# Optimization experiments

Hardware: AMD Instinct MI355X
Metric: run time of the kernel (lower is better)

Reference implementation:

```python
import jax, jax.numpy as jnp
import numpy as np

NEG_INF = -1e30


def setup_inputs() -> dict:
    key = jax.random.key(0)
    k1, k2 = jax.random.split(key)
    B, S, H, D = 2, 2048, 16, 64
    qkv = jax.random.normal(k1, (B, S, 3, H, D), dtype=jnp.float32)
    pos_bias = jax.random.normal(k2, (H, S, S), dtype=jnp.float32)
    return {"qkv": qkv, "pos_bias": pos_bias}


def reference(qkv, pos_bias):
    # qkv: (B, S, 3, H, D); fixed-length path of FlashAttention.forward
    # (key_padding_mask=None, cu_seqlens=None) -> standard per-batch attention
    # with additive per-head positional bias and causal masking.
    B, S, _, H, D = qkv.shape
    q = qkv[:, :, 0]  # (B, S, H, D)
    k = qkv[:, :, 1]
    v = qkv[:, :, 2]
    softmax_scale = 1.0 / jnp.sqrt(jnp.asarray(D, dtype=qkv.dtype))
    # scores: (B, H, S, S)
    scores = jnp.einsum('bshd,bthd->bhst', q, k) * softmax_scale
    scores = scores + pos_bias[None]  # broadcast bias over batch
    # causal mask (query s attends to keys t <= s)
    causal = jnp.tril(jnp.ones((S, S), dtype=bool))
    scores = jnp.where(causal[None, None], scores, NEG_INF)
    attn = jax.nn.softmax(scores, axis=-1)
    # output: (B, S, H, D)
    out = jnp.einsum('bhst,bthd->bshd', attn, v)
    return out
```

## Files before the change

kernel.cpp:

```cpp
#include <hip/hip_runtime.h>

typedef float f32x4 __attribute__((ext_vector_type(4)));
typedef __bf16 bf16x8 __attribute__((ext_vector_type(8)));

#define MFMA16(a, b, c) __builtin_amdgcn_mfma_f32_16x16x32_bf16(a, b, c, 0, 0, 0)

constexpr int S = 2048, H = 16, Dh = 64;
constexpr int BR = 64, BC = 64;
#define NEG_INF_F (-1e30f)

__device__ __forceinline__ void gld16(const __bf16* g, __bf16* l) {
    __builtin_amdgcn_global_load_lds(
        (const __attribute__((address_space(1))) void*)(g),
        (__attribute__((address_space(3))) void*)(l), 16, 0, 0);
}

__global__ __launch_bounds__(256) void prep(const float* __restrict__ qkv,
                                            __bf16* __restrict__ khat,
                                            __bf16* __restrict__ vT)
{
    __shared__ __bf16 vtile[64][72];
    const int tid = threadIdx.x;
    const int bid = blockIdx.x;
    const int tt  = bid & 31;
    const int bh  = bid >> 5;
    const int b   = bh >> 4, h = bh & 15;
    const int t0  = tt * 64;
    const int tr  = tid >> 2, c0 = (tid & 3) * 16;

    const float* kp = qkv + (((size_t)(b * S + t0 + tr) * 3 + 1) * H + h) * Dh + c0;
    const float* vp = qkv + (((size_t)(b * S + t0 + tr) * 3 + 2) * H + h) * Dh + c0;
    f32x4 k0 = *(const f32x4*)(kp + 0), k1 = *(const f32x4*)(kp + 4),
          k2 = *(const f32x4*)(kp + 8), k3 = *(const f32x4*)(kp + 12);
    f32x4 v0 = *(const f32x4*)(vp + 0), v1 = *(const f32x4*)(vp + 4),
          v2 = *(const f32x4*)(vp + 8), v3 = *(const f32x4*)(vp + 12);
    bf16x8 ka, kb, va, vb;
#pragma unroll
    for (int j = 0; j < 4; ++j) {
        ka[j] = (__bf16)k0[j]; ka[4 + j] = (__bf16)k1[j];
        kb[j] = (__bf16)k2[j]; kb[4 + j] = (__bf16)k3[j];
        va[j] = (__bf16)v0[j]; va[4 + j] = (__bf16)v1[j];
        vb[j] = (__bf16)v2[j]; vb[4 + j] = (__bf16)v3[j];
    }
    {
        __bf16* kd = khat + ((size_t)bh * S + t0 + tr) * Dh;
        const int g0 = c0 >> 3, sw = tr & 7;
        *(bf16x8*)(kd + ((( g0    ) ^ sw) << 3)) = ka;
        *(bf16x8*)(kd + (((g0 + 1) ^ sw) << 3)) = kb;
    }
    *(bf16x8*)&vtile[tr][c0]     = va;
    *(bf16x8*)&vtile[tr][c0 + 8] = vb;
    __syncthreads();
    const int d = tid >> 2, tc0 = (tid & 3) * 16;
    bf16x8 x, y;
#pragma unroll
    for (int i = 0; i < 8; ++i) {
        x[i] = vtile[tc0 + i][d];
        y[i] = vtile[tc0 + 8 + i][d];
    }
    __bf16* vd = vT + ((size_t)bh * Dh + d) * S + t0;
    const int h0 = tc0 >> 3, sv = d & 7;
    *(bf16x8*)(vd + ((( h0    ) ^ sv) << 3)) = x;
    *(bf16x8*)(vd + (((h0 + 1) ^ sv) << 3)) = y;
}

__global__ __launch_bounds__(256, 4) void fa_fwd(
    const float* __restrict__ qkv, const float* __restrict__ pb,
    const __bf16* __restrict__ khat, const __bf16* __restrict__ vT,
    float* __restrict__ out)
{
    __shared__ __bf16 klds[64 * 64];
    __shared__ __bf16 vlds[64 * 64];
    __shared__ __bf16 plds[4][16][72];

    const int tid  = threadIdx.x;
    const int wave = tid >> 6;
    const int lane = tid & 63;
    const int quad = lane >> 4;
    const int l16  = lane & 15;

    const int g  = blockIdx.x >> 8;
    const int pp = blockIdx.x & 255;
    const int kk = pp >> 5, hb = pp & 31;
    const int b  = hb & 1, h = hb >> 1;
    const int qt = (g == 0) ? 31 - kk : (g == 1) ? 16 + kk : (g == 2) ? 15 - kk : kk;
    const int q0 = qt * BR;
    const int bh = b * H + h;
    const float scale = 0.125f;

    const int qrow = q0 + wave * 16 + l16;
    const float* qp = qkv + (((size_t)(b * S + qrow) * 3 + 0) * H + h) * Dh;
    bf16x8 qfrag[2];
#pragma unroll
    for (int ks = 0; ks < 2; ++ks) {
        f32x4 a = *(const f32x4*)(qp + ks * 32 + quad * 8);
        f32x4 c = *(const f32x4*)(qp + ks * 32 + quad * 8 + 4);
#pragma unroll
        for (int j = 0; j < 4; ++j) qfrag[ks][j] = (__bf16)a[j];
#pragma unroll
        for (int j = 0; j < 4; ++j) qfrag[ks][4 + j] = (__bf16)c[j];
    }

    const int lrow  = wave * 16 + quad * 4;
    const int myrow = q0 + lrow;
    float l_r[4] = {0.f, 0.f, 0.f, 0.f};
    f32x4 oacc[4];
#pragma unroll
    for (int dt = 0; dt < 4; ++dt) oacc[dt] = (f32x4){0.f, 0.f, 0.f, 0.f};

    const int seg = wave * 2;
    const int lt  = lane >> 3, le = (lane & 7) * 8;
    const __bf16* kg = khat + ((size_t)bh * S + (seg * 8 + lt)) * 64 + le;
    const __bf16* vg = vT   + ((size_t)bh * Dh + seg * 8 + lt) * S + le;
    __bf16* kl = klds + seg * 512;
    __bf16* vl = vlds + seg * 512;

    const float* bb = pb + (size_t)h * S * S + (size_t)myrow * S + l16;
    const int swz = l16 & 7;

    for (int it = 0; it <= qt; ++it) {
        __syncthreads();
        gld16(kg,         kl);
        gld16(kg + 512,   kl + 512);
        gld16(vg,         vl);
        gld16(vg + 8 * S, vl + 512);
        kg += BC * 64; vg += BC;

        float breg[16];
#pragma unroll
        for (int ct = 0; ct < 4; ++ct)
#pragma unroll
            for (int r = 0; r < 4; ++r) breg[ct * 4 + r] = bb[(size_t)r * S + ct * 16];
        bb += BC;
        __syncthreads();

        f32x4 sacc[4];
#pragma unroll
        for (int ct = 0; ct < 4; ++ct) sacc[ct] = (f32x4){0.f, 0.f, 0.f, 0.f};
#pragma unroll
        for (int ct = 0; ct < 4; ++ct) {
#pragma unroll
            for (int ks = 0; ks < 2; ++ks) {
                bf16x8 kf = *(const bf16x8*)&klds[(ct * 16 + l16) * 64 + (((ks * 4 + quad) ^ swz) << 3)];
                sacc[ct] = MFMA16(qfrag[ks], kf, sacc[ct]);
            }
        }

        const bool diag = (it == qt);
#pragma unroll
        for (int ct = 0; ct < 4; ++ct) {
            const int colrel = ct * 16 + l16;
#pragma unroll
            for (int r = 0; r < 4; ++r) {
                float s = fmaf(sacc[ct][r], scale, breg[ct * 4 + r]);
                if (diag && (colrel > lrow + r)) s = NEG_INF_F;
                float p = __expf(s);
                l_r[r] += p;
                plds[wave][quad * 4 + r][colrel] = (__bf16)p;
            }
        }

        bf16x8 pf[2];
#pragma unroll
        for (int ks = 0; ks < 2; ++ks)
            pf[ks] = *(const bf16x8*)&plds[wave][l16][ks * 32 + quad * 8];
#pragma unroll
        for (int dt = 0; dt < 4; ++dt) {
#pragma unroll
            for (int ks = 0; ks < 2; ++ks) {
                bf16x8 vf = *(const bf16x8*)&vlds[(dt * 16 + l16) * 64 + (((ks * 4 + quad) ^ swz) << 3)];
                oacc[dt] = MFMA16(pf[ks], vf, oacc[dt]);
            }
        }
    }

#pragma unroll
    for (int r = 0; r < 4; ++r) {
#pragma unroll
        for (int m = 1; m < 16; m <<= 1) l_r[r] += __shfl_xor(l_r[r], m, 64);
        const float inv = 1.0f / l_r[r];
        float* op = out + (((size_t)(b * S + (myrow + r)) * H) + h) * Dh;
#pragma unroll
        for (int dt = 0; dt < 4; ++dt)
            op[dt * 16 + l16] = oacc[dt][r] * inv;
    }
}

extern "C" void kernel_launch(void* const* d_in, const int* in_sizes, int n_in,
                              void* d_out, int out_size, void* d_ws, size_t ws_size,
                              hipStream_t stream) {
    const float* qkv = (const float*)d_in[0];
    const float* pb  = (const float*)d_in[1];
    float* out       = (float*)d_out;

    constexpr size_t KV_ELEMS = (size_t)2 * H * S * Dh;
    __bf16* khat = (__bf16*)d_ws;
    __bf16* vT   = khat + KV_ELEMS;

    prep<<<dim3(1024), dim3(256), 0, stream>>>(qkv, khat, vT);
    fa_fwd<<<dim3(1024), dim3(256), 0, stream>>>(qkv, pb, khat, vT, out);
}
```

Measured before the change: 404.7 us.

## Double-buffer K/V tiles and bias prefetch with 128-row query blocks

Grows each block to 8 waves covering 128 query rows, so the grid is 512 blocks of 512 threads. K/V tiles in shared memory are now double-buffered and the bias values for the next tile are prefetched into registers while the current tile is computed, which drops one barrier per iteration. The larger query tile lets more waves share each K/V load. In exchange, register pressure rises from holding two bias buffers, and causal load balance gets coarser, with only 512 blocks and the reverse-order pairing now spread over two groups instead of four.

```diff
diff --git a/kernel.cpp b/kernel.cpp
--- a/kernel.cpp
+++ b/kernel.cpp
@@ -6,7 +6,6 @@
 #define MFMA16(a, b, c) __builtin_amdgcn_mfma_f32_16x16x32_bf16(a, b, c, 0, 0, 0)
 
 constexpr int S = 2048, H = 16, Dh = 64;
-constexpr int BR = 64, BC = 64;
 #define NEG_INF_F (-1e30f)
 
 __device__ __forceinline__ void gld16(const __bf16* g, __bf16* l) {
@@ -64,14 +63,14 @@
     *(bf16x8*)(vd + (((h0 + 1) ^ sv) << 3)) = y;
 }
 
-__global__ __launch_bounds__(256, 4) void fa_fwd(
+__global__ __launch_bounds__(512, 4) void fa_fwd(
     const float* __restrict__ qkv, const float* __restrict__ pb,
     const __bf16* __restrict__ khat, const __bf16* __restrict__ vT,
     float* __restrict__ out)
 {
-    __shared__ __bf16 klds[64 * 64];
-    __shared__ __bf16 vlds[64 * 64];
-    __shared__ __bf16 plds[4][16][72];
+    __shared__ __bf16 klds[2][4096];
+    __shared__ __bf16 vlds[2][4096];
+    __shared__ __bf16 plds[8][16][66];
 
     const int tid  = threadIdx.x;
     const int wave = tid >> 6;
@@ -83,9 +82,10 @@
     const int pp = blockIdx.x & 255;
     const int kk = pp >> 5, hb = pp & 31;
     const int b  = hb & 1, h = hb >> 1;
-    const int qt = (g == 0) ? 31 - kk : (g == 1) ? 16 + kk : (g == 2) ? 15 - kk : kk;
-    const int q0 = qt * BR;
-    const int bh = b * H + h;
+    const int qt2 = g ? kk : 15 - kk;
+    const int q0  = qt2 * 128;
+    const int bh  = b * H + h;
+    const int niter = 2 * qt2 + 2;
     const float scale = 0.125f;
 
     const int qrow = q0 + wave * 16 + l16;
@@ -101,38 +101,38 @@
         for (int j = 0; j < 4; ++j) qfrag[ks][4 + j] = (__bf16)c[j];
     }
 
-    const int lrow  = wave * 16 + quad * 4;
-    const int myrow = q0 + lrow;
+    const int myrow = q0 + wave * 16 + quad * 4;
     float l_r[4] = {0.f, 0.f, 0.f, 0.f};
     f32x4 oacc[4];
 #pragma unroll
     for (int dt = 0; dt < 4; ++dt) oacc[dt] = (f32x4){0.f, 0.f, 0.f, 0.f};
 
-    const int seg = wave * 2;
-    const int lt  = lane >> 3, le = (lane & 7) * 8;
-    const __bf16* kg = khat + ((size_t)bh * S + (seg * 8 + lt)) * 64 + le;
-    const __bf16* vg = vT   + ((size_t)bh * Dh + seg * 8 + lt) * S + le;
-    __bf16* kl = klds + seg * 512;
-    __bf16* vl = vlds + seg * 512;
-
-    const float* bb = pb + (size_t)h * S * S + (size_t)myrow * S + l16;
+    const int lt = lane >> 3, le = (lane & 7) * 8;
+    const __bf16* kg = khat + ((size_t)bh * S + wave * 8 + lt) * 64 + le;
+    const __bf16* vg = vT + ((size_t)(bh * Dh + wave * 8 + lt)) * S + le;
+    const float*  bb = pb + (size_t)h * S * S + (size_t)myrow * S + l16;
     const int swz = l16 & 7;
 
-    for (int it = 0; it <= qt; ++it) {
-        __syncthreads();
-        gld16(kg,         kl);
-        gld16(kg + 512,   kl + 512);
-        gld16(vg,         vl);
-        gld16(vg + 8 * S, vl + 512);
-        kg += BC * 64; vg += BC;
-
-        float breg[16];
-#pragma unroll
-        for (int ct = 0; ct < 4; ++ct)
-#pragma unroll
-            for (int r = 0; r < 4; ++r) breg[ct * 4 + r] = bb[(size_t)r * S + ct * 16];
-        bb += BC;
-        __syncthreads();
+    float ba[16], bn[16];
+
+    gld16(kg, &klds[0][wave * 512]);
+    gld16(vg, &vlds[0][wave * 512]);
+#pragma unroll
+    for (int ct = 0; ct < 4; ++ct)
+#pragma unroll
+        for (int r = 0; r < 4; ++r) ba[ct * 4 + r] = bb[(size_t)r * S + ct * 16];
+    __syncthreads();
+
+    auto step = [&](int it, int cb, float* bcur, float* bnext) {
+        if (it + 1 < niter) {
+            gld16(kg + (size_t)(it + 1) * 4096, &klds[cb ^ 1][wave * 512]);
+            gld16(vg + (it + 1) * 64,           &vlds[cb ^ 1][wave * 512]);
+#pragma unroll
+            for (int ct = 0; ct < 4; ++ct)
+#pragma unroll
+                for (int r = 0; r < 4; ++r)
+                    bnext[ct * 4 + r] = bb[(size_t)r * S + (it + 1) * 64 + ct * 16];
+        }
 
         f32x4 sacc[4];
 #pragma unroll
@@ -141,22 +141,22 @@
         for (int ct = 0; ct < 4; ++ct) {
 #pragma unroll
             for (int ks = 0; ks < 2; ++ks) {
-                bf16x8 kf = *(const bf16x8*)&klds[(ct * 16 + l16) * 64 + (((ks * 4 + quad) ^ swz) << 3)];
+                bf16x8 kf = *(const bf16x8*)&klds[cb][(ct * 16 + l16) * 64 + (((ks * 4 + quad) ^ swz) << 3)];
                 sacc[ct] = MFMA16(qfrag[ks], kf, sacc[ct]);
             }
         }
 
-        const bool diag = (it == qt);
+        const bool diag = (it >= niter - 2);
 #pragma unroll
         for (int ct = 0; ct < 4; ++ct) {
-            const int colrel = ct * 16 + l16;
+            const int col = it * 64 + ct * 16 + l16;
 #pragma unroll
             for (int r = 0; r < 4; ++r) {
-                float s = fmaf(sacc[ct][r], scale, breg[ct * 4 + r]);
-                if (diag && (colrel > lrow + r)) s = NEG_INF_F;
-                float p = __expf(s);
+                float s_ = fmaf(sacc[ct][r], scale, bcur[ct * 4 + r]);
+                if (diag && (col > myrow + r)) s_ = NEG_INF_F;
+                float p = __expf(s_);
                 l_r[r] += p;
-                plds[wave][quad * 4 + r][colrel] = (__bf16)p;
+                plds[wave][quad * 4 + r][ct * 16 + l16] = (__bf16)p;
             }
         }
 
@@ -168,10 +168,17 @@
         for (int dt = 0; dt < 4; ++dt) {
 #pragma unroll
             for (int ks = 0; ks < 2; ++ks) {
-                bf16x8 vf = *(const bf16x8*)&vlds[(dt * 16 + l16) * 64 + (((ks * 4 + quad) ^ swz) << 3)];
+                bf16x8 vf = *(const bf16x8*)&vlds[cb][(dt * 16 + l16) * 64 + (((ks * 4 + quad) ^ swz) << 3)];
                 oacc[dt] = MFMA16(pf[ks], vf, oacc[dt]);
             }
         }
+
+        __syncthreads();
+    };
+
+    for (int it = 0; it < niter; it += 2) {
+        step(it,     0, ba, bn);
+        step(it + 1, 1, bn, ba);
     }
 
 #pragma unroll
@@ -198,5 +205,5 @@
     __bf16* vT   = khat + KV_ELEMS;
 
     prep<<<dim3(1024), dim3(256), 0, stream>>>(qkv, khat, vT);
-    fa_fwd<<<dim3(1024), dim3(256), 0, stream>>>(qkv, pb, khat, vT, out);
-}
+    fa_fwd<<<dim3(512), dim3(512), 0, stream>>>(qkv, pb, khat, vT, out);
+}
```

After: 410.6 us. No clear change (+1.4%).
